# Performance work log

Hardware: AMD Instinct MI355X
Metric: run time of the kernel (lower is better)

## Reference

```python
import jax, jax.numpy as jnp
import numpy as np

B, H, S, D = 2, 16, 2048, 64


def setup_inputs() -> dict:
    key = jax.random.key(0)
    kq, kk, kv = jax.random.split(key, 3)
    q = jax.random.normal(kq, (B, H, S, D), dtype=jnp.float32)
    k = jax.random.normal(kk, (B, H, S, D), dtype=jnp.float32)
    v = jax.random.normal(kv, (B, H, S, D), dtype=jnp.float32)
    # causal mask: 1.0 where attention is DISALLOWED (strictly upper triangle)
    mask = jnp.triu(jnp.ones((S, S), dtype=jnp.float32), k=1)[None, None, :, :]
    return {"k": k, "q": q, "v": v, "mask": mask}


def reference(k, q, v, mask):
    d_k = jnp.asarray(k.shape[-1], dtype=jnp.float32)
    # scores: [B, H, S, S]
    scores = jnp.einsum("bhqd,bhkd->bhqk", q, k) / jnp.sqrt(d_k)
    scores = scores + mask * (-1e9)
    weights = jax.nn.softmax(scores, axis=-1)
    # attention output: [B, H, S, D]
    return jnp.einsum("bhqk,bhkd->bhqd", weights, v)
```

## Files before the change

kernel.cpp:

```cpp
#include <hip/hip_runtime.h>
#include <hip/hip_bf16.h>

typedef unsigned short ushort_t;
typedef __attribute__((ext_vector_type(8))) short v8s;
typedef __attribute__((ext_vector_type(4))) float v4f;

#define SEQ   2048
#define DH    64
#define BK    32
#define KSTR  72
#define VSTR  40
#define NHEADS 32
#define GBYTES 19456
#define HELEMS 131072

#if __has_builtin(__builtin_amdgcn_exp2f)
#define EXP2(x) __builtin_amdgcn_exp2f(x)
#else
#define EXP2(x) exp2f(x)
#endif

__device__ __forceinline__ unsigned pkbf(float lo, float hi) {
    __hip_bfloat162 h = __float22bfloat162_rn(make_float2(lo, hi));
    union { __hip_bfloat162 h; unsigned u; } c; c.h = h; return c.u;
}

__device__ __forceinline__ v8s load8_bf_scaled(const float* p, float sc) {
    float4 a = *(const float4*)p;
    float4 b = *(const float4*)(p + 4);
    union { v8s v; unsigned u[4]; } t;
    t.u[0] = pkbf(a.x * sc, a.y * sc);
    t.u[1] = pkbf(a.z * sc, a.w * sc);
    t.u[2] = pkbf(b.x * sc, b.y * sc);
    t.u[3] = pkbf(b.z * sc, b.w * sc);
    return t.v;
}

__device__ __forceinline__ void process_tile_T(
    int kb, int myq0, int quad, int l15,
    v8s qa0, v8s qa1,
    v8s ka00, v8s ka01, v8s ka10, v8s ka11,
    v8s vb0, v8s vb1, v8s vb2, v8s vb3,
    v4f& a0, v4f& a1, v4f& a2, v4f& a3, float& ls)
{
    const v4f z = {0.f, 0.f, 0.f, 0.f};
    __builtin_amdgcn_s_setprio(1);
    v4f s0 = __builtin_amdgcn_mfma_f32_16x16x32_bf16(ka00, qa0, z, 0, 0, 0);
    s0     = __builtin_amdgcn_mfma_f32_16x16x32_bf16(ka01, qa1, s0, 0, 0, 0);
    v4f s1 = __builtin_amdgcn_mfma_f32_16x16x32_bf16(ka10, qa0, z, 0, 0, 0);
    s1     = __builtin_amdgcn_mfma_f32_16x16x32_bf16(ka11, qa1, s1, 0, 0, 0);
    __builtin_amdgcn_s_setprio(0);

    float p0[4], p1[4];
    if (kb + BK <= myq0) {
        #pragma unroll
        for (int r = 0; r < 4; ++r) { p0[r] = EXP2(s0[r]); p1[r] = EXP2(s1[r]); }
    } else {
        const int qrow = myq0 + l15;
        #pragma unroll
        for (int r = 0; r < 4; ++r) {
            p0[r] = (kb + 4 * quad + r      <= qrow) ? EXP2(s0[r]) : 0.f;
            p1[r] = (kb + 16 + 4 * quad + r <= qrow) ? EXP2(s1[r]) : 0.f;
        }
    }
    #pragma unroll
    for (int r = 0; r < 4; ++r) ls += p0[r] + p1[r];

    union { v8s v; unsigned u[4]; } pa;
    pa.u[0] = pkbf(p0[0], p0[1]); pa.u[1] = pkbf(p0[2], p0[3]);
    pa.u[2] = pkbf(p1[0], p1[1]); pa.u[3] = pkbf(p1[2], p1[3]);
    __builtin_amdgcn_s_setprio(1);
    a0 = __builtin_amdgcn_mfma_f32_16x16x32_bf16(pa.v, vb0, a0, 0, 0, 0);
    a1 = __builtin_amdgcn_mfma_f32_16x16x32_bf16(pa.v, vb1, a1, 0, 0, 0);
    a2 = __builtin_amdgcn_mfma_f32_16x16x32_bf16(pa.v, vb2, a2, 0, 0, 0);
    a3 = __builtin_amdgcn_mfma_f32_16x16x32_bf16(pa.v, vb3, a3, 0, 0, 0);
    __builtin_amdgcn_s_setprio(0);
}

__global__ __launch_bounds__(256, 8)
void attn_prep(const float* __restrict__ K, const float* __restrict__ V,
               ushort_t* __restrict__ Kf, ushort_t* __restrict__ Vf) {
    const int u = blockIdx.x * 256 + threadIdx.x;
    if (u < 524288) {
        const int lane = u & 63;
        const int l15  = lane & 15, quad = lane >> 4;
        const int f    = (u >> 6) & 3;
        const int kt   = (u >> 8) & 63;
        const int head = u >> 14;
        const int row  = kt * 32 + ((f & 2) ? 16 : 0) + l15;
        const int col  = ((f & 1) ? 32 : 0) + quad * 8;
        const float* src = K + ((size_t)head * SEQ + row) * DH + col;
        float4 a = *(const float4*)src;
        float4 b = *(const float4*)(src + 4);
        union { v8s v; unsigned w[4]; } t;
        t.w[0] = pkbf(a.x, a.y); t.w[1] = pkbf(a.z, a.w);
        t.w[2] = pkbf(b.x, b.y); t.w[3] = pkbf(b.z, b.w);
        *(v8s*)(Kf + (size_t)u * 8) = t.v;
    } else {
        const int q    = u - 524288;
        const int lane = q & 63;
        const int l15  = lane & 15, qd = lane >> 4;
        const int b    = (q >> 6) & 3;
        const int kt   = (q >> 8) & 63;
        const int head = q >> 14;
        const float* vsrc = V + ((size_t)head * SEQ + kt * 32) * DH + (l15 + 16 * b);
        float x[8];
        #pragma unroll
        for (int j = 0; j < 8; ++j) {
            const int kpos = (j < 4) ? (4 * qd + j) : (16 + 4 * qd + (j - 4));
            x[j] = vsrc[(size_t)kpos * DH];
        }
        union { v8s v; unsigned w[4]; } t;
        t.w[0] = pkbf(x[0], x[1]); t.w[1] = pkbf(x[2], x[3]);
        t.w[2] = pkbf(x[4], x[5]); t.w[3] = pkbf(x[6], x[7]);
        *(v8s*)(Vf + (size_t)q * 8) = t.v;
    }
}

__global__ __launch_bounds__(64, 2)
void attn_causal_wave(const ushort_t* __restrict__ Kf,
                      const float* __restrict__ Qg,
                      const ushort_t* __restrict__ Vf,
                      float* __restrict__ Og) {
    const int i    = blockIdx.x;
    const int head = i & 31;
    const int c    = 63 - (i >> 5);
    const int qb   = c * 32;
    const int lane = threadIdx.x;
    const int l15  = lane & 15;
    const int quad = lane >> 4;
    const int myqA = qb, myqB = qb + 16;
    const size_t hb = (size_t)head * SEQ * DH;

    const float QSC = 0.125f * 1.4426950408889634f;
    v8s qaA0, qaA1, qaB0, qaB1;
    {
        const float* qpA = Qg + hb + (size_t)(myqA + l15) * DH + quad * 8;
        const float* qpB = Qg + hb + (size_t)(myqB + l15) * DH + quad * 8;
        qaA0 = load8_bf_scaled(qpA, QSC); qaA1 = load8_bf_scaled(qpA + 32, QSC);
        qaB0 = load8_bf_scaled(qpB, QSC); qaB1 = load8_bf_scaled(qpB + 32, QSC);
    }

    v4f aA0 = {0.f,0.f,0.f,0.f}, aA1 = aA0, aA2 = aA0, aA3 = aA0;
    v4f aB0 = aA0, aB1 = aA0, aB2 = aA0, aB3 = aA0;
    float lsA = 0.f, lsB = 0.f;

    const ushort_t* kf = Kf + (size_t)head * HELEMS + lane * 8;
    const ushort_t* vf = Vf + (size_t)head * HELEMS + lane * 8;
    const int nt = c + 1;

    union U { v8s v; uint4 u; };
    U k0c, k1c, k2c, k3c, v0c, v1c, v2c, v3c;
    {
        k0c.u = *(const uint4*)(kf);        k1c.u = *(const uint4*)(kf + 512);
        k2c.u = *(const uint4*)(kf + 1024); k3c.u = *(const uint4*)(kf + 1536);
        v0c.u = *(const uint4*)(vf);        v1c.u = *(const uint4*)(vf + 512);
        v2c.u = *(const uint4*)(vf + 1024); v3c.u = *(const uint4*)(vf + 1536);
    }

    for (int kt = 0; kt < nt; ++kt) {
        U k0n, k1n, k2n, k3n, v0n, v1n, v2n, v3n;
        const bool havenext = (kt + 1 < nt);
        if (havenext) {
            const ushort_t* kp = kf + (size_t)(kt + 1) * 2048;
            const ushort_t* vp = vf + (size_t)(kt + 1) * 2048;
            k0n.u = *(const uint4*)(kp);        k1n.u = *(const uint4*)(kp + 512);
            k2n.u = *(const uint4*)(kp + 1024); k3n.u = *(const uint4*)(kp + 1536);
            v0n.u = *(const uint4*)(vp);        v1n.u = *(const uint4*)(vp + 512);
            v2n.u = *(const uint4*)(vp + 1024); v3n.u = *(const uint4*)(vp + 1536);
        }

        const int kb = kt * BK;
        process_tile_T(kb, myqA, quad, l15, qaA0, qaA1,
                       k0c.v, k1c.v, k2c.v, k3c.v,
                       v0c.v, v1c.v, v2c.v, v3c.v,
                       aA0, aA1, aA2, aA3, lsA);
        process_tile_T(kb, myqB, quad, l15, qaB0, qaB1,
                       k0c.v, k1c.v, k2c.v, k3c.v,
                       v0c.v, v1c.v, v2c.v, v3c.v,
                       aB0, aB1, aB2, aB3, lsB);

        if (havenext) {
            k0c = k0n; k1c = k1n; k2c = k2n; k3c = k3n;
            v0c = v0n; v1c = v1n; v2c = v2n; v3c = v3n;
        }
    }

    lsA += __shfl_xor(lsA, 16); lsA += __shfl_xor(lsA, 32);
    lsB += __shfl_xor(lsB, 16); lsB += __shfl_xor(lsB, 32);
    #pragma unroll
    for (int r = 0; r < 4; ++r) {
        const float invA = 1.0f / __shfl(lsA, 4 * quad + r);
        const float invB = 1.0f / __shfl(lsB, 4 * quad + r);
        float* opA = Og + hb + (size_t)(myqA + 4 * quad + r) * DH + l15;
        float* opB = Og + hb + (size_t)(myqB + 4 * quad + r) * DH + l15;
        opA[0]  = aA0[r] * invA; opA[16] = aA1[r] * invA;
        opA[32] = aA2[r] * invA; opA[48] = aA3[r] * invA;
        opB[0]  = aB0[r] * invB; opB[16] = aB1[r] * invB;
        opB[32] = aB2[r] * invB; opB[48] = aB3[r] * invB;
    }
}

__global__ __launch_bounds__(512, 4)
void attn_causal_dual(const float* __restrict__ Kg,
                      const float* __restrict__ Qg,
                      const float* __restrict__ Vg,
                      float* __restrict__ Og) {
    __shared__ alignas(16) unsigned char smem[2][GBYTES];

    const int i    = blockIdx.x;
    const int head = i & 31;
    const int j    = i >> 5;
    const int qt   = (j < 16) ? (31 - j) : (j - 16);
    const int qb   = qt * 64;
    const int tid  = threadIdx.x;
    const int w    = tid >> 6;
    const int grp  = w >> 2;
    const int wg   = w & 3;
    const int lane = tid & 63;
    const int l15  = lane & 15;
    const int quad = lane >> 4;

    const int niter = qt + 1;
    const int ktlo  = grp ? niter : 0;

    const int myq0 = qb + wg * 16, qmax = myq0 + 15;
    const size_t hb = (size_t)head * SEQ * DH;

    const float QSC = 0.125f * 1.4426950408889634f;
    v8s qa0, qa1;
    {
        const float* qp = Qg + hb + (size_t)(myq0 + l15) * DH + quad * 8;
        qa0 = load8_bf_scaled(qp, QSC);  qa1 = load8_bf_scaled(qp + 32, QSC);
    }

    v4f a0 = {0.f,0.f,0.f,0.f}, a1 = a0, a2 = a0, a3 = a0;
    float ls = 0.f;

    const int stid    = tid & 255;
    const int sk_kpos = stid >> 3;
    const int sk_d    = (stid & 7) * 8;
    const int sv_d    = stid & 63;

    const float* kbase  = Kg + hb + (size_t)sk_kpos * DH + sk_d;
    const float* vbaseA = Vg + hb + (size_t)(4 * wg) * DH + sv_d;
    const float* vbaseB = Vg + hb + (size_t)(16 + 4 * wg) * DH + sv_d;

    ushort_t* KtB = (ushort_t*)(smem[grp]);
    ushort_t* VtB = (ushort_t*)(smem[grp] + 9216);
    ushort_t* kdst0 = KtB + sk_kpos * KSTR + sk_d;
    ushort_t* vdst0 = VtB + sv_d * VSTR + 8 * wg;
    const int KOFS = BK * KSTR;
    const int VOFS = DH * VSTR;

    {
        const size_t t0 = (size_t)ktlo * BK * DH;
        float4 k0 = *(const float4*)(kbase + t0);
        float4 k1 = *(const float4*)(kbase + t0 + 4);
        float va[4], vb[4];
        #pragma unroll
        for (int m = 0; m < 4; ++m) {
            va[m] = vbaseA[t0 + (size_t)m * DH];
            vb[m] = vbaseB[t0 + (size_t)m * DH];
        }
        union { v8s v; unsigned u[4]; } kc, vc;
        kc.u[0] = pkbf(k0.x, k0.y); kc.u[1] = pkbf(k0.z, k0.w);
        kc.u[2] = pkbf(k1.x, k1.y); kc.u[3] = pkbf(k1.z, k1.w);
        vc.u[0] = pkbf(va[0], va[1]); vc.u[1] = pkbf(va[2], va[3]);
        vc.u[2] = pkbf(vb[0], vb[1]); vc.u[3] = pkbf(vb[2], vb[3]);
        *(v8s*)kdst0 = kc.v;
        *(v8s*)vdst0 = vc.v;
    }
    __syncthreads();

    for (int it = 0; it < niter; ++it) {
        const int kt  = ktlo + it;
        const int cur = it & 1;
        const bool havenext = (it + 1 < niter);

        float4 nk0, nk1; float nva[4], nvb[4];
        if (havenext) {
            const size_t toff = (size_t)(kt + 1) * BK * DH;
            nk0 = *(const float4*)(kbase + toff);
            nk1 = *(const float4*)(kbase + toff + 4);
            #pragma unroll
            for (int m = 0; m < 4; ++m) {
                nva[m] = vbaseA[toff + (size_t)m * DH];
                nvb[m] = vbaseB[toff + (size_t)m * DH];
            }
        }

        const int kb = kt * BK;
        if (kb <= qmax) {
            const ushort_t* KB = KtB + (cur ? KOFS : 0);
            const ushort_t* VB = VtB + (cur ? VOFS : 0);
            union { v8s v; uint4 u; } ka00, ka01, ka10, ka11, vb0, vb1, vb2, vb3;
            ka00.u = *(const uint4*)&KB[(l15)      * KSTR      + quad * 8];
            ka01.u = *(const uint4*)&KB[(l15)      * KSTR + 32 + quad * 8];
            ka10.u = *(const uint4*)&KB[(16 + l15) * KSTR      + quad * 8];
            ka11.u = *(const uint4*)&KB[(16 + l15) * KSTR + 32 + quad * 8];
            vb0.u  = *(const uint4*)&VB[(l15)      * VSTR + quad * 8];
            vb1.u  = *(const uint4*)&VB[(16 + l15) * VSTR + quad * 8];
            vb2.u  = *(const uint4*)&VB[(32 + l15) * VSTR + quad * 8];
            vb3.u  = *(const uint4*)&VB[(48 + l15) * VSTR + quad * 8];

            process_tile_T(kb, myq0, quad, l15, qa0, qa1,
                           ka00.v, ka01.v, ka10.v, ka11.v,
                           vb0.v, vb1.v, vb2.v, vb3.v,
                           a0, a1, a2, a3, ls);
        }

        if (havenext) {
            union { v8s v; unsigned u[4]; } kc, vc;
            kc.u[0] = pkbf(nk0.x, nk0.y); kc.u[1] = pkbf(nk0.z, nk0.w);
            kc.u[2] = pkbf(nk1.x, nk1.y); kc.u[3] = pkbf(nk1.z, nk1.w);
            vc.u[0] = pkbf(nva[0], nva[1]); vc.u[1] = pkbf(nva[2], nva[3]);
            vc.u[2] = pkbf(nvb[0], nvb[1]); vc.u[3] = pkbf(nvb[2], nvb[3]);
            const int nxt = cur ^ 1;
            *(v8s*)(kdst0 + (nxt ? KOFS : 0)) = kc.v;
            *(v8s*)(vdst0 + (nxt ? VOFS : 0)) = vc.v;
        }

        __syncthreads();
    }

    ls += __shfl_xor(ls, 16); ls += __shfl_xor(ls, 32);

    float* Ps2 = (float*)smem[0];
    float* Lp2 = (float*)smem[1];
    if (grp == 1) {
        #pragma unroll
        for (int r = 0; r < 4; ++r) {
            const int row = wg * 16 + 4 * quad + r;
            float* pr = Ps2 + row * 68 + l15;
            pr[0] = a0[r]; pr[16] = a1[r]; pr[32] = a2[r]; pr[48] = a3[r];
        }
        if (lane < 16) Lp2[wg * 16 + l15] = ls;
    }
    __syncthreads();
    if (grp == 0) {
        const float lst = ls + Lp2[wg * 16 + l15];
        #pragma unroll
        for (int r = 0; r < 4; ++r) {
            const float inv = 1.0f / __shfl(lst, 4 * quad + r);
            const int row = wg * 16 + 4 * quad + r;
            const float* pr = Ps2 + row * 68 + l15;
            float* op = Og + hb + (size_t)(qb + row) * DH + l15;
            op[0]  = (a0[r] + pr[0])  * inv;
            op[16] = (a1[r] + pr[16]) * inv;
            op[32] = (a2[r] + pr[32]) * inv;
            op[48] = (a3[r] + pr[48]) * inv;
        }
    }
}

extern "C" void kernel_launch(void* const* d_in, const int* in_sizes, int n_in,
                              void* d_out, int out_size, void* d_ws, size_t ws_size,
                              hipStream_t stream) {
    const float* K = (const float*)d_in[0];
    const float* Q = (const float*)d_in[1];
    const float* V = (const float*)d_in[2];
    float* O = (float*)d_out;

    const size_t img_elems = (size_t)NHEADS * HELEMS;
    const size_t need = 2 * img_elems * sizeof(ushort_t);

    if (ws_size >= need) {
        ushort_t* Kf = (ushort_t*)d_ws;
        ushort_t* Vf = Kf + img_elems;
        attn_prep<<<dim3(4096), 256, 0, stream>>>(K, V, Kf, Vf);
        attn_causal_wave<<<dim3(2048), 64, 0, stream>>>(Kf, Q, Vf, O);
    } else {
        attn_causal_dual<<<dim3(1024), 512, 0, stream>>>(K, Q, V, O);
    }
}
```

Baseline: 141.4 us.

## Split key-tile loop across two waves per block with LDS reduction

Each 32-query block now runs with two wavefronts that each handle half of the causal key tiles. Partial accumulators and row sums from the second wave are written to shared memory and merged by the first wave before normalising and storing. This halves the serial loop length per wave, which shortens the critical path for long diagonal rows. In exchange it adds a block barrier and LDS traffic, and it drops the explicit register double-buffered prefetch of K/V tiles. The merge relies on no running-max rescaling, so the partial sums combine by plain addition.

```diff
diff --git a/kernel.cpp b/kernel.cpp
--- a/kernel.cpp
+++ b/kernel.cpp
@@ -117,20 +117,30 @@
     }
 }
 
-__global__ __launch_bounds__(64, 2)
-void attn_causal_wave(const ushort_t* __restrict__ Kf,
-                      const float* __restrict__ Qg,
-                      const ushort_t* __restrict__ Vf,
-                      float* __restrict__ Og) {
+__global__ __launch_bounds__(128, 4)
+void attn_causal_wave2(const ushort_t* __restrict__ Kf,
+                       const float* __restrict__ Qg,
+                       const ushort_t* __restrict__ Vf,
+                       float* __restrict__ Og) {
+    __shared__ alignas(16) float Ps[32 * 68];
+    __shared__ float Lp[32];
+
     const int i    = blockIdx.x;
     const int head = i & 31;
     const int c    = 63 - (i >> 5);
     const int qb   = c * 32;
-    const int lane = threadIdx.x;
+    const int tid  = threadIdx.x;
+    const int grp  = tid >> 6;
+    const int lane = tid & 63;
     const int l15  = lane & 15;
     const int quad = lane >> 4;
     const int myqA = qb, myqB = qb + 16;
     const size_t hb = (size_t)head * SEQ * DH;
+
+    const int nt   = c + 1;
+    const int n0   = (nt + 1) >> 1;
+    const int ktlo = grp ? n0 : 0;
+    const int kthi = grp ? nt : n0;
 
     const float QSC = 0.125f * 1.4426950408889634f;
     v8s qaA0, qaA1, qaB0, qaB1;
@@ -147,57 +157,65 @@
 
     const ushort_t* kf = Kf + (size_t)head * HELEMS + lane * 8;
     const ushort_t* vf = Vf + (size_t)head * HELEMS + lane * 8;
-    const int nt = c + 1;
-
-    union U { v8s v; uint4 u; };
-    U k0c, k1c, k2c, k3c, v0c, v1c, v2c, v3c;
-    {
-        k0c.u = *(const uint4*)(kf);        k1c.u = *(const uint4*)(kf + 512);
-        k2c.u = *(const uint4*)(kf + 1024); k3c.u = *(const uint4*)(kf + 1536);
-        v0c.u = *(const uint4*)(vf);        v1c.u = *(const uint4*)(vf + 512);
-        v2c.u = *(const uint4*)(vf + 1024); v3c.u = *(const uint4*)(vf + 1536);
-    }
-
-    for (int kt = 0; kt < nt; ++kt) {
-        U k0n, k1n, k2n, k3n, v0n, v1n, v2n, v3n;
-        const bool havenext = (kt + 1 < nt);
-        if (havenext) {
-            const ushort_t* kp = kf + (size_t)(kt + 1) * 2048;
-            const ushort_t* vp = vf + (size_t)(kt + 1) * 2048;
-            k0n.u = *(const uint4*)(kp);        k1n.u = *(const uint4*)(kp + 512);
-            k2n.u = *(const uint4*)(kp + 1024); k3n.u = *(const uint4*)(kp + 1536);
-            v0n.u = *(const uint4*)(vp);        v1n.u = *(const uint4*)(vp + 512);
-            v2n.u = *(const uint4*)(vp + 1024); v3n.u = *(const uint4*)(vp + 1536);
-        }
+
+    for (int kt = ktlo; kt < kthi; ++kt) {
+        const ushort_t* kp = kf + (size_t)kt * 2048;
+        const ushort_t* vp = vf + (size_t)kt * 2048;
+        union { v8s v; uint4 u; } k0, k1, k2, k3, v0, v1, v2, v3;
+        k0.u = *(const uint4*)(kp);        k1.u = *(const uint4*)(kp + 512);
+        k2.u = *(const uint4*)(kp + 1024); k3.u = *(const uint4*)(kp + 1536);
+        v0.u = *(const uint4*)(vp);        v1.u = *(const uint4*)(vp + 512);
+        v2.u = *(const uint4*)(vp + 1024); v3.u = *(const uint4*)(vp + 1536);
 
         const int kb = kt * BK;
         process_tile_T(kb, myqA, quad, l15, qaA0, qaA1,
-                       k0c.v, k1c.v, k2c.v, k3c.v,
-                       v0c.v, v1c.v, v2c.v, v3c.v,
+                       k0.v, k1.v, k2.v, k3.v,
+                       v0.v, v1.v, v2.v, v3.v,
                        aA0, aA1, aA2, aA3, lsA);
         process_tile_T(kb, myqB, quad, l15, qaB0, qaB1,
-                       k0c.v, k1c.v, k2c.v, k3c.v,
-                       v0c.v, v1c.v, v2c.v, v3c.v,
+                       k0.v, k1.v, k2.v, k3.v,
+                       v0.v, v1.v, v2.v, v3.v,
                        aB0, aB1, aB2, aB3, lsB);
-
-        if (havenext) {
-            k0c = k0n; k1c = k1n; k2c = k2n; k3c = k3n;
-            v0c = v0n; v1c = v1n; v2c = v2n; v3c = v3n;
-        }
     }
 
     lsA += __shfl_xor(lsA, 16); lsA += __shfl_xor(lsA, 32);
     lsB += __shfl_xor(lsB, 16); lsB += __shfl_xor(lsB, 32);
-    #pragma unroll
-    for (int r = 0; r < 4; ++r) {
-        const float invA = 1.0f / __shfl(lsA, 4 * quad + r);
-        const float invB = 1.0f / __shfl(lsB, 4 * quad + r);
-        float* opA = Og + hb + (size_t)(myqA + 4 * quad + r) * DH + l15;
-        float* opB = Og + hb + (size_t)(myqB + 4 * quad + r) * DH + l15;
-        opA[0]  = aA0[r] * invA; opA[16] = aA1[r] * invA;
-        opA[32] = aA2[r] * invA; opA[48] = aA3[r] * invA;
-        opB[0]  = aB0[r] * invB; opB[16] = aB1[r] * invB;
-        opB[32] = aB2[r] * invB; opB[48] = aB3[r] * invB;
+
+    if (grp == 1) {
+        #pragma unroll
+        for (int r = 0; r < 4; ++r) {
+            const int rowA = 4 * quad + r;
+            const int rowB = 16 + 4 * quad + r;
+            float* prA = Ps + rowA * 68 + l15;
+            float* prB = Ps + rowB * 68 + l15;
+            prA[0] = aA0[r]; prA[16] = aA1[r]; prA[32] = aA2[r]; prA[48] = aA3[r];
+            prB[0] = aB0[r]; prB[16] = aB1[r]; prB[32] = aB2[r]; prB[48] = aB3[r];
+        }
+        if (lane < 16) { Lp[l15] = lsA; Lp[16 + l15] = lsB; }
+    }
+    __syncthreads();
+    if (grp == 0) {
+        const float lstA = lsA + Lp[l15];
+        const float lstB = lsB + Lp[16 + l15];
+        #pragma unroll
+        for (int r = 0; r < 4; ++r) {
+            const float invA = 1.0f / __shfl(lstA, 4 * quad + r);
+            const float invB = 1.0f / __shfl(lstB, 4 * quad + r);
+            const int rowA = 4 * quad + r;
+            const int rowB = 16 + 4 * quad + r;
+            const float* prA = Ps + rowA * 68 + l15;
+            const float* prB = Ps + rowB * 68 + l15;
+            float* opA = Og + hb + (size_t)(myqA + rowA) * DH + l15;
+            float* opB = Og + hb + (size_t)(myqB + rowB - 16) * DH + l15;
+            opA[0]  = (aA0[r] + prA[0])  * invA;
+            opA[16] = (aA1[r] + prA[16]) * invA;
+            opA[32] = (aA2[r] + prA[32]) * invA;
+            opA[48] = (aA3[r] + prA[48]) * invA;
+            opB[0]  = (aB0[r] + prB[0])  * invB;
+            opB[16] = (aB1[r] + prB[16]) * invB;
+            opB[32] = (aB2[r] + prB[32]) * invB;
+            opB[48] = (aB3[r] + prB[48]) * invB;
+        }
     }
 }
 
@@ -369,7 +387,7 @@
         ushort_t* Kf = (ushort_t*)d_ws;
         ushort_t* Vf = Kf + img_elems;
         attn_prep<<<dim3(4096), 256, 0, stream>>>(K, V, Kf, Vf);
-        attn_causal_wave<<<dim3(2048), 64, 0, stream>>>(Kf, Q, Vf, O);
+        attn_causal_wave2<<<dim3(2048), 128, 0, stream>>>(Kf, Q, Vf, O);
     } else {
         attn_causal_dual<<<dim3(1024), 512, 0, stream>>>(K, Q, V, O);
     }
```

After: 130.8 us. -7.6%, faster.
